# Kernel optimization log

Hardware: AMD Instinct MI355X
Metric: run time of the kernel (lower is better)

Reference implementation:

```python
import jax, jax.numpy as jnp
import numpy as np

N_NODE, NODE_DIM = 20000, 128
N_EDGE, EDGE_DIM = 40000, 16
BN_EPS = 1e-5


def _bn(x, gamma, beta):
    # training-mode BatchNorm1d: batch statistics, biased variance
    mu = jnp.mean(x, axis=0)
    var = jnp.mean((x - mu) ** 2, axis=0)
    return (x - mu) * jax.lax.rsqrt(var + BN_EPS) * gamma + beta


def setup_inputs() -> dict:
    key = jax.random.key(0)
    ks = jax.random.split(key, 16)
    D = NODE_DIM

    def lin(k, fan_in, fan_out):
        s = 1.0 / np.sqrt(fan_in)
        return jax.random.uniform(k, (fan_in, fan_out), jnp.float32, -s, s)

    inp = {
        "node": jax.random.normal(ks[0], (N_NODE, D), jnp.float32),
        "edge_index": jax.random.randint(ks[1], (N_EDGE, 2), 0, N_NODE),
        "edge": jax.random.normal(ks[2], (N_EDGE, EDGE_DIM), jnp.float32),
        "hidden": jax.random.normal(ks[3], (1, N_NODE, D), jnp.float32),
        # encoder: LinearBn(edge_dim,256) ReLU LinearBn(256,256) ReLU LinearBn(256,128) ReLU LinearBn(128,D*D)
        "W1": lin(ks[4], EDGE_DIM, 256), "g1": jnp.ones((256,)), "be1": jnp.zeros((256,)),
        "W2": lin(ks[5], 256, 256), "g2": jnp.ones((256,)), "be2": jnp.zeros((256,)),
        "W3": lin(ks[6], 256, 128), "g3": jnp.ones((128,)), "be3": jnp.zeros((128,)),
        "W4": lin(ks[7], 128, D * D), "g4": jnp.ones((D * D,)), "be4": jnp.zeros((D * D,)),
        "bias": jax.random.uniform(ks[8], (D,), jnp.float32, -1.0 / np.sqrt(D), 1.0 / np.sqrt(D)),
        # GRU weights, torch layout [3D, D]
        "W_ih": lin(ks[9], D, 3 * D).T, "W_hh": lin(ks[10], D, 3 * D).T,
        "b_ih": jax.random.uniform(ks[11], (3 * D,), jnp.float32, -1.0 / np.sqrt(D), 1.0 / np.sqrt(D)),
        "b_hh": jax.random.uniform(ks[12], (3 * D,), jnp.float32, -1.0 / np.sqrt(D), 1.0 / np.sqrt(D)),
    }
    return inp


def reference(node, edge_index, edge, hidden,
              W1, g1, be1, W2, g2, be2, W3, g3, be3, W4, g4, be4,
              bias, W_ih, W_hh, b_ih, b_hh):
    num_node, D = node.shape
    src = edge_index[:, 0]
    dst = edge_index[:, 1]

    # edge encoder -> per-edge [D, D] mixing matrix
    h = jax.nn.relu(_bn(edge @ W1, g1, be1))
    h = jax.nn.relu(_bn(h @ W2, g2, be2))
    h = jax.nn.relu(_bn(h @ W3, g3, be3))
    ew = _bn(h @ W4, g4, be4).reshape(-1, D, D)  # [E, D, D]

    # gather + per-edge 1xD @ DxD
    x_i = node[src]                               # [E, D]
    message = jnp.einsum('ed,edf->ef', x_i, ew)   # [E, D]

    # scatter-mean over destination nodes
    sums = jax.ops.segment_sum(message, dst, num_segments=num_node)
    cnt = jax.ops.segment_sum(jnp.ones((message.shape[0],), message.dtype), dst, num_segments=num_node)
    mean = sums / jnp.maximum(cnt, 1.0)[:, None]

    msg = jax.nn.relu(mean + bias)

    # GRU cell (seq_len=1, batch=num_node), torch gate order r,z,n
    h0 = hidden[0]
    gi = msg @ W_ih.T + b_ih
    gh = h0 @ W_hh.T + b_hh
    gi_r, gi_z, gi_n = jnp.split(gi, 3, axis=-1)
    gh_r, gh_z, gh_n = jnp.split(gh, 3, axis=-1)
    r = jax.nn.sigmoid(gi_r + gh_r)
    z = jax.nn.sigmoid(gi_z + gh_z)
    n = jnp.tanh(gi_n + r * gh_n)
    h1 = (1.0 - z) * n + z * h0

    return h1, h1[None]
```

## Files before the change

### kernel.cpp

```cpp
#include <hip/hip_runtime.h>
#include <cstdint>
#include <cstddef>

#define N_NODE_C 20000
#define N_EDGE_C 40000
#define BN_EPS_F 1e-5f
#define NSB 160
#define H3T_STRIDE 40064

typedef __attribute__((ext_vector_type(8))) short bf16x8;
typedef __attribute__((ext_vector_type(16))) float f32x16;

__device__ __forceinline__ ushort f2bf(float x) {
  unsigned u = __float_as_uint(x);
  unsigned r = u + 0x7fffu + ((u >> 16) & 1u);
  return (ushort)(r >> 16);
}
__device__ __forceinline__ float bf2f(ushort b) {
  return __uint_as_float(((unsigned)b) << 16);
}

__device__ __forceinline__ void gl_lds16(const ushort* g, ushort* l) {
  __builtin_amdgcn_global_load_lds(
      (const __attribute__((address_space(1))) unsigned int*)(g),
      (__attribute__((address_space(3))) unsigned int*)(l), 16, 0, 0);
}

__global__ __launch_bounds__(256) void k_transpose_gru(
    const float* __restrict__ Wih, const float* __restrict__ Whh,
    float* __restrict__ WihT, float* __restrict__ WhhT) {
  int i = blockIdx.x * 256 + threadIdx.x;
  int which = i / 49152;
  int idx = i - which * 49152;
  int k = idx / 384, o = idx - k * 384;
  float v = which ? Whh[o * 128 + k] : Wih[o * 128 + k];
  if (which) WhhT[idx] = v; else WihT[idx] = v;
}

__global__ __launch_bounds__(256) void k_edge_w1(
    const float* __restrict__ edge, const float* __restrict__ W1,
    float* __restrict__ y1) {
  __shared__ float el[16][16];
  int e0 = blockIdx.x * 16;
  int t = threadIdx.x;
  el[t >> 4][t & 15] = edge[(size_t)e0 * 16 + t];
  __syncthreads();
  float w[16];
#pragma unroll
  for (int k = 0; k < 16; ++k) w[k] = W1[k * 256 + t];
#pragma unroll 4
  for (int e = 0; e < 16; ++e) {
    float acc = 0.f;
#pragma unroll
    for (int k = 0; k < 16; ++k) acc = fmaf(el[e][k], w[k], acc);
    y1[(size_t)(e0 + e) * 256 + t] = acc;
  }
}

__global__ __launch_bounds__(256) void k_colstats(
    const float* __restrict__ y, int E, int J,
    double* __restrict__ sum, double* __restrict__ sumsq) {
  int t = threadIdx.x;
  int rpi = 256 / J;
  int col = t & (J - 1);
  int rof = t / J;
  double s = 0.0, q = 0.0;
  for (int r = blockIdx.x * rpi + rof; r < E; r += gridDim.x * rpi) {
    float v = y[(size_t)r * J + col];
    s += v;
    q += (double)v * (double)v;
  }
  atomicAdd(&sum[col], s);
  atomicAdd(&sumsq[col], q);
}

__global__ void k_finalize(const double* __restrict__ sum,
                           const double* __restrict__ sumsq,
                           const float* __restrict__ g,
                           const float* __restrict__ be,
                           float* __restrict__ a, float* __restrict__ b,
                           int J, double invE) {
  int j = threadIdx.x;
  if (j < J) {
    double mu = sum[j] * invE;
    double var = sumsq[j] * invE - mu * mu;
    float rstd = (float)(1.0 / sqrt(var + 1e-5));
    float aa = g[j] * rstd;
    a[j] = aa;
    b[j] = be[j] - (float)mu * aa;
  }
}

template <int MODE>
__global__ __launch_bounds__(256) void k_gemm(
    const float* __restrict__ A, const float* __restrict__ B,
    float* __restrict__ C, int M, int K, int N,
    const float* __restrict__ ta, const float* __restrict__ tb,
    const float* __restrict__ bias) {
  __shared__ float At[32][64];
  __shared__ float Bt[32][128];
  int mb = blockIdx.x * 64, nb = blockIdx.y * 128;
  int tid = threadIdx.x;
  int tr = tid >> 5, tc = tid & 31;
  float acc[8][4];
#pragma unroll
  for (int i = 0; i < 8; ++i)
#pragma unroll
    for (int j = 0; j < 4; ++j) acc[i][j] = 0.f;
  int arow = tid >> 2, akc = (tid & 3) * 8;
  int bkr = tid >> 3, bcol = (tid & 7) * 16;
  for (int k0 = 0; k0 < K; k0 += 32) {
    {
      int gr = mb + arow;
      float vv[8];
      if (gr < M) {
        float4 v0 = *(const float4*)&A[(size_t)gr * K + k0 + akc];
        float4 v1 = *(const float4*)&A[(size_t)gr * K + k0 + akc + 4];
        vv[0] = v0.x; vv[1] = v0.y; vv[2] = v0.z; vv[3] = v0.w;
        vv[4] = v1.x; vv[5] = v1.y; vv[6] = v1.z; vv[7] = v1.w;
      } else {
#pragma unroll
        for (int u = 0; u < 8; ++u) vv[u] = 0.f;
      }
#pragma unroll
      for (int u = 0; u < 8; ++u) {
        float x = vv[u];
        if (MODE == 1) {
          int k = k0 + akc + u;
          x = fmaxf(fmaf(x, ta[k], tb[k]), 0.f);
        }
        At[akc + u][arow] = x;
      }
    }
    {
      const float* src = &B[(size_t)(k0 + bkr) * N + nb + bcol];
      float4* d = (float4*)&Bt[bkr][bcol];
      d[0] = ((const float4*)src)[0];
      d[1] = ((const float4*)src)[1];
      d[2] = ((const float4*)src)[2];
      d[3] = ((const float4*)src)[3];
    }
    __syncthreads();
#pragma unroll 8
    for (int kk = 0; kk < 32; ++kk) {
      float4 a0 = *(float4*)&At[kk][tr * 8];
      float4 a1 = *(float4*)&At[kk][tr * 8 + 4];
      float4 b0 = *(float4*)&Bt[kk][tc * 4];
      float av[8] = {a0.x, a0.y, a0.z, a0.w, a1.x, a1.y, a1.z, a1.w};
      float bv[4] = {b0.x, b0.y, b0.z, b0.w};
#pragma unroll
      for (int i = 0; i < 8; ++i)
#pragma unroll
        for (int j = 0; j < 4; ++j)
          acc[i][j] = fmaf(av[i], bv[j], acc[i][j]);
    }
    __syncthreads();
  }
#pragma unroll
  for (int i = 0; i < 8; ++i) {
    int gr = mb + tr * 8 + i;
    if (gr < M) {
      int oc = nb + tc * 4;
      float4 o;
      o.x = acc[i][0]; o.y = acc[i][1]; o.z = acc[i][2]; o.w = acc[i][3];
      if (bias) {
        o.x += bias[oc]; o.y += bias[oc + 1];
        o.z += bias[oc + 2]; o.w += bias[oc + 3];
      }
      *(float4*)&C[(size_t)gr * N + oc] = o;
    }
  }
}

__global__ __launch_bounds__(256) void k_bnrelu_inplace(
    float* __restrict__ y, const float* __restrict__ a,
    const float* __restrict__ b, int n, int J) {
  int i = blockIdx.x * 256 + threadIdx.x;
  if (i < n) {
    int c = i & (J - 1);
    y[i] = fmaxf(fmaf(y[i], a[c], b[c]), 0.f);
  }
}

__global__ __launch_bounds__(256) void k_cov_partials(
    const float* __restrict__ h3, float* __restrict__ Spart,
    float* __restrict__ hbarP) {
  __shared__ float hl[2][128];
  int b = blockIdx.x;
  int t = threadIdx.x;
  int tr = t >> 4, tc = t & 15;
  float acc[8][8];
#pragma unroll
  for (int i = 0; i < 8; ++i)
#pragma unroll
    for (int j = 0; j < 8; ++j) acc[i][j] = 0.f;
  float cs = 0.f;
  int r0 = b * 250;
  for (int rs = 0; rs < 250; rs += 2) {
    hl[t >> 7][t & 127] = h3[(size_t)(r0 + rs + (t >> 7)) * 128 + (t & 127)];
    __syncthreads();
#pragma unroll
    for (int rr = 0; rr < 2; ++rr) {
      float a0[8], b0[8];
#pragma unroll
      for (int i = 0; i < 8; ++i) a0[i] = hl[rr][tr * 8 + i];
#pragma unroll
      for (int j = 0; j < 8; ++j) b0[j] = hl[rr][tc * 8 + j];
#pragma unroll
      for (int i = 0; i < 8; ++i)
#pragma unroll
        for (int j = 0; j < 8; ++j)
          acc[i][j] = fmaf(a0[i], b0[j], acc[i][j]);
    }
    if (t < 128) cs += hl[0][t] + hl[1][t];
    __syncthreads();
  }
  float* sp = &Spart[(size_t)b * 16384];
#pragma unroll
  for (int i = 0; i < 8; ++i)
#pragma unroll
    for (int j = 0; j < 8; j += 4) {
      float4 o;
      o.x = acc[i][j]; o.y = acc[i][j + 1];
      o.z = acc[i][j + 2]; o.w = acc[i][j + 3];
      *(float4*)&sp[(tr * 8 + i) * 128 + tc * 8 + j] = o;
    }
  if (t < 128) hbarP[b * 128 + t] = cs;
}

__global__ void k_hbar(const float* __restrict__ hbarP,
                       double* __restrict__ hbarD, float* __restrict__ hbarF) {
  int t = threadIdx.x;
  double s = 0.0;
  for (int b = 0; b < NSB; ++b) s += (double)hbarP[b * 128 + t];
  s *= (1.0 / 40000.0);
  hbarD[t] = s;
  hbarF[t] = (float)s;
}

__global__ __launch_bounds__(256) void k_cov(
    const float* __restrict__ Spart, const double* __restrict__ hbarD,
    float* __restrict__ Cov) {
  int i = blockIdx.x * 256 + threadIdx.x;
  int k = i >> 7, l = i & 127;
  double s = 0.0;
  for (int b = 0; b < NSB; ++b) s += (double)Spart[(size_t)b * 16384 + i];
  Cov[i] = (float)(s * (1.0 / 40000.0) - hbarD[k] * hbarD[l]);
}

__global__ __launch_bounds__(256) void k_covW4(
    const float* __restrict__ Cov, const float* __restrict__ W4,
    float* __restrict__ U) {
  __shared__ float cl[8][128];
  int bk = blockIdx.x & 15, bj = blockIdx.x >> 4;
  int k0 = bk * 8, j0 = bj * 2048;
  int t = threadIdx.x;
  {
    float4 v = *(const float4*)&Cov[(size_t)(k0 + (t >> 5)) * 128 + (t & 31) * 4];
    *(float4*)&cl[t >> 5][(t & 31) * 4] = v;
  }
  __syncthreads();
  for (int ji = 0; ji < 8; ++ji) {
    int j = j0 + ji * 256 + t;
    float acc[8];
#pragma unroll
    for (int i = 0; i < 8; ++i) acc[i] = 0.f;
#pragma unroll 4
    for (int l = 0; l < 128; ++l) {
      float w = W4[(size_t)l * 16384 + j];
#pragma unroll
      for (int i = 0; i < 8; ++i) acc[i] = fmaf(cl[i][l], w, acc[i]);
    }
#pragma unroll
    for (int i = 0; i < 8; ++i) U[(size_t)(k0 + i) * 16384 + j] = acc[i];
  }
}

__global__ __launch_bounds__(256) void k_a4nb4(
    const float* __restrict__ W4, const float* __restrict__ U,
    const float* __restrict__ hbarF, const float* __restrict__ g4,
    const float* __restrict__ be4, float* __restrict__ a4,
    float* __restrict__ nb4) {
  __shared__ float hb[128];
  int t = threadIdx.x;
  if (t < 128) hb[t] = hbarF[t];
  __syncthreads();
  int j = blockIdx.x * 256 + t;
  float macc = 0.f, vacc = 0.f;
#pragma unroll 4
  for (int k = 0; k < 128; ++k) {
    float w = W4[(size_t)k * 16384 + j];
    macc = fmaf(hb[k], w, macc);
    vacc = fmaf(w, U[(size_t)k * 16384 + j], vacc);
  }
  float aa = g4[j] * (1.0f / sqrtf(vacc + BN_EPS_F));
  a4[j] = aa;
  nb4[j] = be4[j] - macc * aa;
}

__global__ __launch_bounds__(256) void k_split_node(
    const float* __restrict__ node, ushort* __restrict__ nH,
    ushort* __restrict__ nL) {
  int i = blockIdx.x * 256 + threadIdx.x;
  int base = i * 4;
  float4 v = *(const float4*)&node[base];
  ushort4 h, lo;
  float x;
  x = v.x; h.x = f2bf(x); lo.x = f2bf(x - bf2f(h.x));
  x = v.y; h.y = f2bf(x); lo.y = f2bf(x - bf2f(h.y));
  x = v.z; h.z = f2bf(x); lo.z = f2bf(x - bf2f(h.z));
  x = v.w; h.w = f2bf(x); lo.w = f2bf(x - bf2f(h.w));
  *(ushort4*)&nH[base] = h;
  *(ushort4*)&nL[base] = lo;
}

__global__ __launch_bounds__(256) void k_h3T(const float* __restrict__ y3,
                                             float* __restrict__ h3T) {
  __shared__ float tile[32][33];
  int bx = blockIdx.x;
  int by = blockIdx.y;
  int tx = threadIdx.x & 31, ty = threadIdx.x >> 5;
#pragma unroll
  for (int i = 0; i < 4; ++i) {
    int e = bx * 32 + ty + 8 * i;
    float v = (e < 40000) ? y3[(size_t)e * 128 + by * 32 + tx] : 0.f;
    tile[ty + 8 * i][tx] = v;
  }
  __syncthreads();
#pragma unroll
  for (int i = 0; i < 4; ++i) {
    int kk = by * 32 + ty + 8 * i;
    h3T[(size_t)kk * H3T_STRIDE + bx * 32 + tx] = tile[tx][ty + 8 * i];
  }
}

__global__ __launch_bounds__(256) void k_buildB2(
    const float* __restrict__ W4, const float* __restrict__ a4,
    const float* __restrict__ nb4, ushort* __restrict__ B2) {
  int tid = blockIdx.x * 256 + threadIdx.x;
  int k = tid >> 14;
  int rem = tid & 16383;
  int H = rem >> 13;
  int rem2 = rem & 8191;
  int j = rem2 & 7;
  int lane = (rem2 >> 3) & 63;
  int cgg = (rem2 >> 9) & 1;
  int dstep = rem2 >> 10;
  int d = dstep * 16 + (lane >> 5) * 8 + j;
  int f = H * 64 + cgg * 32 + (lane & 31);
  int df = d * 128 + f;
  float v;
  if (k < 128) v = W4[(size_t)k * 16384 + df] * a4[df];
  else v = nb4[df];
  ushort hi = f2bf(v);
  ushort lo = f2bf(v - bf2f(hi));
  size_t base = ((size_t)(k * 2 + H)) * 16384 +
                (size_t)((dstep * 2 + cgg) * 2) * 512 + lane * 8 + j;
  B2[base] = hi;
  B2[base + 512] = lo;
}

__global__ __launch_bounds__(512) void k_biggemm3(
    const ushort* __restrict__ nodeH, const ushort* __restrict__ B2,
    const float* __restrict__ h3T, const int* __restrict__ eidx,
    float* __restrict__ msum, float* __restrict__ cnt) {
  __shared__ ushort Bl[2][8192];
  __shared__ int sidx[128], didx[128];
  const int t = threadIdx.x;
  const int e0 = blockIdx.x * 128;
  const int H = blockIdx.y;
  const int KZ = blockIdx.z;
  const int K0 = KZ ? 65 : 0;
  const int KN = KZ ? 64 : 65;
  const int w = t >> 6;
  const int l = t & 63;
  const int rg = w >> 1;
  const int cg = w & 1;
  const int dg = l >> 5;

  if (t < 256) {
    int e = e0 + (t >> 1);
    int v = (e < 40000) ? eidx[(size_t)e * 2 + (t & 1)] : 0;
    if (t & 1) didx[t >> 1] = v; else sidx[t >> 1] = v;
  }
  {
    const size_t cb = (size_t)(K0 * 2 + H) * 16384;
#pragma unroll
    for (int j = 0; j < 2; ++j) {
      int flat = t + j * 512;
      gl_lds16(B2 + cb + (size_t)(flat >> 6) * 1024 + (flat & 63) * 8,
               &Bl[0][flat * 8]);
    }
  }
  __syncthreads();

  const int myrow = rg * 32 + (l & 31);
  const int esrc = sidx[myrow];
  bf16x8 xh[8];
  {
    const ushort* ph = nodeH + (size_t)esrc * 128 + dg * 8;
#pragma unroll
    for (int d2 = 0; d2 < 8; ++d2) xh[d2] = *(const bf16x8*)(ph + d2 * 16);
  }

  f32x16 msg;
#pragma unroll
  for (int r = 0; r < 16; ++r) msg[r] = 0.f;

  for (int ki = 0; ki < KN; ++ki) {
    const int kc = K0 + ki;
    const int buf = ki & 1;
    if (ki + 1 < KN) {
      const size_t cb = (size_t)((kc + 1) * 2 + H) * 16384;
#pragma unroll
      for (int j = 0; j < 2; ++j) {
        int flat = t + j * 512;
        gl_lds16(B2 + cb + (size_t)(flat >> 6) * 1024 + (flat & 63) * 8,
                 &Bl[buf ^ 1][flat * 8]);
      }
    }
    float4 hv[4];
    if (kc < 128) {
      const float* hb = h3T + (size_t)kc * H3T_STRIDE + e0 + rg * 32 + 4 * dg;
#pragma unroll
      for (int q = 0; q < 4; ++q) hv[q] = *(const float4*)(hb + q * 8);
    } else {
#pragma unroll
      for (int q = 0; q < 4; ++q) hv[q] = make_float4(1.f, 1.f, 1.f, 1.f);
    }
    f32x16 u;
#pragma unroll
    for (int r = 0; r < 16; ++r) u[r] = 0.f;
    const ushort* bbase = &Bl[buf][0];
#pragma unroll
    for (int d2 = 0; d2 < 8; ++d2) {
      bf16x8 bh = *(const bf16x8*)(bbase + (d2 * 2 + cg) * 512 + l * 8);
      u = __builtin_amdgcn_mfma_f32_32x32x16_bf16(xh[d2], bh, u, 0, 0, 0);
    }
#pragma unroll
    for (int r = 0; r < 16; ++r) {
      float hval = ((const float*)&hv[r >> 2])[r & 3];
      msg[r] = fmaf(hval, u[r], msg[r]);
    }
    __syncthreads();
  }

  const int fbase = H * 64 + cg * 32 + (l & 31);
#pragma unroll
  for (int r = 0; r < 16; ++r) {
    int lrow = rg * 32 + (r & 3) + 8 * (r >> 2) + 4 * dg;
    int ge = e0 + lrow;
    if (ge < 40000)
      atomicAdd(&msum[(size_t)didx[lrow] * 128 + fbase], msg[r]);
  }
  if (KZ == 0 && H == 0 && t < 128) {
    int ge = e0 + t;
    if (ge < 40000) atomicAdd(&cnt[didx[t]], 1.0f);
  }
}

__global__ __launch_bounds__(256) void k_msg(
    const float* __restrict__ msum, const float* __restrict__ cnt,
    const float* __restrict__ bias, float* __restrict__ msg) {
  int i = blockIdx.x * 256 + threadIdx.x;
  int nn = i >> 7, f = i & 127;
  float m = msum[i] / fmaxf(cnt[nn], 1.0f);
  msg[i] = fmaxf(m + bias[f], 0.f);
}

__global__ __launch_bounds__(256) void k_gru(
    const float* __restrict__ gi, const float* __restrict__ gh,
    const float* __restrict__ h0, float* __restrict__ out) {
  int i = blockIdx.x * 256 + threadIdx.x;
  int nn = i >> 7, f = i & 127;
  size_t base = (size_t)nn * 384;
  float ir = gi[base + f], hr = gh[base + f];
  float iz = gi[base + 128 + f], hz = gh[base + 128 + f];
  float in_ = gi[base + 256 + f], hn = gh[base + 256 + f];
  float r = 1.f / (1.f + expf(-(ir + hr)));
  float z = 1.f / (1.f + expf(-(iz + hz)));
  float n = tanhf(in_ + r * hn);
  float h1 = (1.f - z) * n + z * h0[i];
  out[i] = h1;
  out[2560000 + i] = h1;
}

extern "C" void kernel_launch(void* const* d_in, const int* in_sizes, int n_in,
                              void* d_out, int out_size, void* d_ws,
                              size_t ws_size, hipStream_t stream) {
  (void)in_sizes; (void)n_in; (void)out_size; (void)ws_size;
  const float* node = (const float*)d_in[0];
  const int* eidx = (const int*)d_in[1];
  const float* edge = (const float*)d_in[2];
  const float* hidden = (const float*)d_in[3];
  const float* W1 = (const float*)d_in[4];
  const float* g1 = (const float*)d_in[5];
  const float* be1 = (const float*)d_in[6];
  const float* W2 = (const float*)d_in[7];
  const float* g2 = (const float*)d_in[8];
  const float* be2 = (const float*)d_in[9];
  const float* W3 = (const float*)d_in[10];
  const float* g3 = (const float*)d_in[11];
  const float* be3 = (const float*)d_in[12];
  const float* W4 = (const float*)d_in[13];
  const float* g4 = (const float*)d_in[14];
  const float* be4 = (const float*)d_in[15];
  const float* bias = (const float*)d_in[16];
  const float* Wih = (const float*)d_in[17];
  const float* Whh = (const float*)d_in[18];
  const float* bih = (const float*)d_in[19];
  const float* bhh = (const float*)d_in[20];
  float* out = (float*)d_out;

  double* d64 = (double*)d_ws;
  double* sum1 = d64 + 0;
  double* sq1 = d64 + 256;
  double* sum2 = d64 + 512;
  double* sq2 = d64 + 768;
  double* sum3 = d64 + 1024;
  double* sq3 = d64 + 1152;
  double* hbarD = d64 + 1280;
  float* F = (float*)(d64 + 1536);

  size_t o = 0;
  float* y1 = F + o;   o += 10240000;
  float* y2 = F + o;   o += 10240000;
  float* y3 = F + o;   o += 5120000;
  float* B2f = F + o;  o += 2113536;
  float* msum = F + o; o += 2560000;
  float* cnt = F + o;  o += 20000;
  float* msg = F + o;  o += 2560000;
  float* WihT = F + o; o += 49152;
  float* WhhT = F + o; o += 49152;
  float* Cov = F + o;  o += 16384;
  float* a4 = F + o;   o += 16384;
  float* nb4 = F + o;  o += 16384;
  float* a1 = F + o;   o += 256;
  float* b1 = F + o;   o += 256;
  float* a2 = F + o;   o += 256;
  float* b2 = F + o;   o += 256;
  float* a3 = F + o;   o += 128;
  float* b3 = F + o;   o += 128;
  float* hbarF = F + o; o += 128;
  float* Spart = y1;
  float* U = y1 + 2621440;
  float* gi = y1 + 2560000;
  float* h3T = y2;
  float* gh = y2;
  float* hbarP = y2 + 7680000;
  ushort* nodeH = (ushort*)msg;
  ushort* nodeL = ((ushort*)msg) + 2560000;
  ushort* B2 = (ushort*)B2f;

  hipMemsetAsync(d_ws, 0, 12288, stream);
  hipMemsetAsync(msum, 0, (2560000 + 20000) * sizeof(float), stream);

  k_transpose_gru<<<384, 256, 0, stream>>>(Wih, Whh, WihT, WhhT);
  k_split_node<<<2500, 256, 0, stream>>>(node, nodeH, nodeL);

  k_edge_w1<<<2500, 256, 0, stream>>>(edge, W1, y1);
  k_colstats<<<256, 256, 0, stream>>>(y1, 40000, 256, sum1, sq1);
  k_finalize<<<1, 256, 0, stream>>>(sum1, sq1, g1, be1, a1, b1, 256, 1.0 / 40000.0);
  k_gemm<1><<<dim3(625, 2), 256, 0, stream>>>(y1, W2, y2, 40000, 256, 256, a1, b1, nullptr);
  k_colstats<<<256, 256, 0, stream>>>(y2, 40000, 256, sum2, sq2);
  k_finalize<<<1, 256, 0, stream>>>(sum2, sq2, g2, be2, a2, b2, 256, 1.0 / 40000.0);
  k_gemm<1><<<dim3(625, 1), 256, 0, stream>>>(y2, W3, y3, 40000, 256, 128, a2, b2, nullptr);
  k_colstats<<<256, 256, 0, stream>>>(y3, 40000, 128, sum3, sq3);
  k_finalize<<<1, 256, 0, stream>>>(sum3, sq3, g3, be3, a3, b3, 128, 1.0 / 40000.0);
  k_bnrelu_inplace<<<20000, 256, 0, stream>>>(y3, a3, b3, 5120000, 128);

  k_h3T<<<dim3(1252, 4), 256, 0, stream>>>(y3, h3T);

  k_cov_partials<<<NSB, 256, 0, stream>>>(y3, Spart, hbarP);
  k_hbar<<<1, 128, 0, stream>>>(hbarP, hbarD, hbarF);
  k_cov<<<64, 256, 0, stream>>>(Spart, hbarD, Cov);
  k_covW4<<<128, 256, 0, stream>>>(Cov, W4, U);
  k_a4nb4<<<64, 256, 0, stream>>>(W4, U, hbarF, g4, be4, a4, nb4);
  k_buildB2<<<8256, 256, 0, stream>>>(W4, a4, nb4, B2);

  k_biggemm3<<<dim3(313, 2, 2), 512, 0, stream>>>(nodeH, B2, h3T, eidx,
                                                  msum, cnt);

  k_msg<<<10000, 256, 0, stream>>>(msum, cnt, bias, msg);
  k_gemm<0><<<dim3(313, 3), 256, 0, stream>>>(msg, WihT, gi, 20000, 128, 384, nullptr, nullptr, bih);
  k_gemm<0><<<dim3(313, 3), 256, 0, stream>>>(hidden, WhhT, gh, 20000, 128, 384, nullptr, nullptr, bhh);
  k_gru<<<10000, 256, 0, stream>>>(gi, gh, hidden, out);
}
```

Baseline: 875.8 us.

## Move encoder and GRU GEMMs to split-bf16 MFMA, drop low plane in big GEMM

Replaces the fp32 SIMT tiled GEMMs (encoder layers 2 and 3, GRU input and hidden projections) with MFMA 32x32x16 bf16 kernels. These use hi/lo bf16 splitting of both operands (three MFMAs per k-step) to keep near-fp32 accuracy, with new pack kernels that fuse the BN+ReLU prologue into the A split. It also removes the low-precision correction plane from the B2 edge-weight operand of the big message GEMM, halving its load traffic at some accuracy cost. The extra pack passes add memory traffic and launches.

```diff
diff --git a/kernel.cpp b/kernel.cpp
--- a/kernel.cpp
+++ b/kernel.cpp
@@ -24,17 +24,6 @@
   __builtin_amdgcn_global_load_lds(
       (const __attribute__((address_space(1))) unsigned int*)(g),
       (__attribute__((address_space(3))) unsigned int*)(l), 16, 0, 0);
-}
-
-__global__ __launch_bounds__(256) void k_transpose_gru(
-    const float* __restrict__ Wih, const float* __restrict__ Whh,
-    float* __restrict__ WihT, float* __restrict__ WhhT) {
-  int i = blockIdx.x * 256 + threadIdx.x;
-  int which = i / 49152;
-  int idx = i - which * 49152;
-  int k = idx / 384, o = idx - k * 384;
-  float v = which ? Whh[o * 128 + k] : Wih[o * 128 + k];
-  if (which) WhhT[idx] = v; else WihT[idx] = v;
 }
 
 __global__ __launch_bounds__(256) void k_edge_w1(
@@ -88,87 +77,6 @@
     float aa = g[j] * rstd;
     a[j] = aa;
     b[j] = be[j] - (float)mu * aa;
-  }
-}
-
-template <int MODE>
-__global__ __launch_bounds__(256) void k_gemm(
-    const float* __restrict__ A, const float* __restrict__ B,
-    float* __restrict__ C, int M, int K, int N,
-    const float* __restrict__ ta, const float* __restrict__ tb,
-    const float* __restrict__ bias) {
-  __shared__ float At[32][64];
-  __shared__ float Bt[32][128];
-  int mb = blockIdx.x * 64, nb = blockIdx.y * 128;
-  int tid = threadIdx.x;
-  int tr = tid >> 5, tc = tid & 31;
-  float acc[8][4];
-#pragma unroll
-  for (int i = 0; i < 8; ++i)
-#pragma unroll
-    for (int j = 0; j < 4; ++j) acc[i][j] = 0.f;
-  int arow = tid >> 2, akc = (tid & 3) * 8;
-  int bkr = tid >> 3, bcol = (tid & 7) * 16;
-  for (int k0 = 0; k0 < K; k0 += 32) {
-    {
-      int gr = mb + arow;
-      float vv[8];
-      if (gr < M) {
-        float4 v0 = *(const float4*)&A[(size_t)gr * K + k0 + akc];
-        float4 v1 = *(const float4*)&A[(size_t)gr * K + k0 + akc + 4];
-        vv[0] = v0.x; vv[1] = v0.y; vv[2] = v0.z; vv[3] = v0.w;
-        vv[4] = v1.x; vv[5] = v1.y; vv[6] = v1.z; vv[7] = v1.w;
-      } else {
-#pragma unroll
-        for (int u = 0; u < 8; ++u) vv[u] = 0.f;
-      }
-#pragma unroll
-      for (int u = 0; u < 8; ++u) {
-        float x = vv[u];
-        if (MODE == 1) {
-          int k = k0 + akc + u;
-          x = fmaxf(fmaf(x, ta[k], tb[k]), 0.f);
-        }
-        At[akc + u][arow] = x;
-      }
-    }
-    {
-      const float* src = &B[(size_t)(k0 + bkr) * N + nb + bcol];
-      float4* d = (float4*)&Bt[bkr][bcol];
-      d[0] = ((const float4*)src)[0];
-      d[1] = ((const float4*)src)[1];
-      d[2] = ((const float4*)src)[2];
-      d[3] = ((const float4*)src)[3];
-    }
-    __syncthreads();
-#pragma unroll 8
-    for (int kk = 0; kk < 32; ++kk) {
-      float4 a0 = *(float4*)&At[kk][tr * 8];
-      float4 a1 = *(float4*)&At[kk][tr * 8 + 4];
-      float4 b0 = *(float4*)&Bt[kk][tc * 4];
-      float av[8] = {a0.x, a0.y, a0.z, a0.w, a1.x, a1.y, a1.z, a1.w};
-      float bv[4] = {b0.x, b0.y, b0.z, b0.w};
-#pragma unroll
-      for (int i = 0; i < 8; ++i)
-#pragma unroll
-        for (int j = 0; j < 4; ++j)
-          acc[i][j] = fmaf(av[i], bv[j], acc[i][j]);
-    }
-    __syncthreads();
-  }
-#pragma unroll
-  for (int i = 0; i < 8; ++i) {
-    int gr = mb + tr * 8 + i;
-    if (gr < M) {
-      int oc = nb + tc * 4;
-      float4 o;
-      o.x = acc[i][0]; o.y = acc[i][1]; o.z = acc[i][2]; o.w = acc[i][3];
-      if (bias) {
-        o.x += bias[oc]; o.y += bias[oc + 1];
-        o.z += bias[oc + 2]; o.w += bias[oc + 3];
-      }
-      *(float4*)&C[(size_t)gr * N + oc] = o;
-    }
   }
 }
 
@@ -352,12 +260,110 @@
   float v;
   if (k < 128) v = W4[(size_t)k * 16384 + df] * a4[df];
   else v = nb4[df];
+  B2[(size_t)(k * 2 + H) * 8192 + rem2] = f2bf(v);
+}
+
+template <int TRANSPOSED>
+__global__ __launch_bounds__(256) void k_packW(
+    const float* __restrict__ W, int Nd32, int ldw, ushort* __restrict__ out) {
+  int tid = blockIdx.x * 256 + threadIdx.x;
+  int within = tid & 511;
+  int g = tid >> 9;
+  int nt = g % Nd32, kt = g / Nd32;
+  int lane = within >> 3, j = within & 7;
+  int k = kt * 16 + (lane >> 5) * 8 + j;
+  int n = nt * 32 + (lane & 31);
+  float v = TRANSPOSED ? W[(size_t)n * ldw + k] : W[(size_t)k * ldw + n];
   ushort hi = f2bf(v);
   ushort lo = f2bf(v - bf2f(hi));
-  size_t base = ((size_t)(k * 2 + H)) * 16384 +
-                (size_t)((dstep * 2 + cgg) * 2) * 512 + lane * 8 + j;
-  B2[base] = hi;
-  B2[base + 512] = lo;
+  out[((size_t)g * 2 + 0) * 512 + within] = hi;
+  out[((size_t)g * 2 + 1) * 512 + within] = lo;
+}
+
+template <int MODE>
+__global__ __launch_bounds__(256) void k_splitA(
+    const float* __restrict__ A, int M, int Kd16,
+    const float* __restrict__ ta, const float* __restrict__ tb,
+    ushort* __restrict__ out) {
+  int tid = blockIdx.x * 256 + threadIdx.x;
+  int lane = tid & 63;
+  int g = tid >> 6;
+  int kt = g % Kd16, m32 = g / Kd16;
+  int row = m32 * 32 + (lane & 31);
+  int kbase = kt * 16 + (lane >> 5) * 8;
+  float v[8];
+  if (row < M) {
+    const float* src = A + (size_t)row * (Kd16 * 16) + kbase;
+    float4 v0 = ((const float4*)src)[0];
+    float4 v1 = ((const float4*)src)[1];
+    v[0] = v0.x; v[1] = v0.y; v[2] = v0.z; v[3] = v0.w;
+    v[4] = v1.x; v[5] = v1.y; v[6] = v1.z; v[7] = v1.w;
+  } else {
+#pragma unroll
+    for (int u = 0; u < 8; ++u) v[u] = 0.f;
+  }
+  ushort hi[8], lo[8];
+#pragma unroll
+  for (int u = 0; u < 8; ++u) {
+    float x = v[u];
+    if (MODE == 1) {
+      int k = kbase + u;
+      x = fmaxf(fmaf(x, ta[k], tb[k]), 0.f);
+    }
+    hi[u] = f2bf(x);
+    lo[u] = f2bf(x - bf2f(hi[u]));
+  }
+  size_t obase = ((size_t)g * 2) * 512 + lane * 8;
+  *(ushort4*)&out[obase] = make_ushort4(hi[0], hi[1], hi[2], hi[3]);
+  *(ushort4*)&out[obase + 4] = make_ushort4(hi[4], hi[5], hi[6], hi[7]);
+  *(ushort4*)&out[obase + 512] = make_ushort4(lo[0], lo[1], lo[2], lo[3]);
+  *(ushort4*)&out[obase + 516] = make_ushort4(lo[4], lo[5], lo[6], lo[7]);
+}
+
+template <int KD16, int HAS_BIAS>
+__global__ __launch_bounds__(512) void k_mfgemm(
+    const ushort* __restrict__ Apk, const ushort* __restrict__ Bpk,
+    float* __restrict__ C, int M, int Nd32, const float* __restrict__ bias) {
+  __shared__ ushort Bl[KD16 * 4 * 512];
+  const int t = threadIdx.x;
+  const int mb = blockIdx.x, nb = blockIdx.y;
+  const int w = t >> 6, l = t & 63;
+  const int rg = w >> 1, cg = w & 1, dg = l >> 5;
+  constexpr int passes = (KD16 * 4 * 64) / 512;
+#pragma unroll
+  for (int p = 0; p < passes; ++p) {
+    int flat = t + p * 512;
+    int blk = flat >> 6;
+    int off = (flat & 63) * 8;
+    int kt = blk >> 2, cgg = (blk >> 1) & 1, plane = blk & 1;
+    size_t srcb = ((size_t)(kt * Nd32 + nb * 2 + cgg) * 2 + plane) * 512 + off;
+    gl_lds16(Bpk + srcb, &Bl[blk * 512 + off]);
+  }
+  __syncthreads();
+  f32x16 u;
+#pragma unroll
+  for (int r = 0; r < 16; ++r) u[r] = 0.f;
+  const int m32base = mb * 4 + rg;
+#pragma unroll
+  for (int kt = 0; kt < KD16; ++kt) {
+    const ushort* ap = Apk + ((size_t)(m32base * KD16 + kt) * 2) * 512 + l * 8;
+    bf16x8 ah = *(const bf16x8*)ap;
+    bf16x8 al = *(const bf16x8*)(ap + 512);
+    const ushort* bp = &Bl[(kt * 4 + cg * 2) * 512 + l * 8];
+    bf16x8 bh = *(const bf16x8*)bp;
+    bf16x8 bl2 = *(const bf16x8*)(bp + 512);
+    u = __builtin_amdgcn_mfma_f32_32x32x16_bf16(ah, bh, u, 0, 0, 0);
+    u = __builtin_amdgcn_mfma_f32_32x32x16_bf16(ah, bl2, u, 0, 0, 0);
+    u = __builtin_amdgcn_mfma_f32_32x32x16_bf16(al, bh, u, 0, 0, 0);
+  }
+  const int N = Nd32 * 32;
+  const int col = nb * 64 + cg * 32 + (l & 31);
+  const float bv = HAS_BIAS ? bias[col] : 0.f;
+#pragma unroll
+  for (int r = 0; r < 16; ++r) {
+    int row = mb * 128 + rg * 32 + (r & 3) + 8 * (r >> 2) + 4 * dg;
+    if (row < M) C[(size_t)row * N + col] = u[r] + bv;
+  }
 }
 
 __global__ __launch_bounds__(512) void k_biggemm3(
@@ -384,12 +390,11 @@
     if (t & 1) didx[t >> 1] = v; else sidx[t >> 1] = v;
   }
   {
-    const size_t cb = (size_t)(K0 * 2 + H) * 16384;
-#pragma unroll
-    for (int j = 0; j < 2; ++j) {
-      int flat = t + j * 512;
-      gl_lds16(B2 + cb + (size_t)(flat >> 6) * 1024 + (flat & 63) * 8,
-               &Bl[0][flat * 8]);
+    const size_t cb = (size_t)(K0 * 2 + H) * 8192;
+#pragma unroll
+    for (int jj = 0; jj < 2; ++jj) {
+      int flat = t + jj * 512;
+      gl_lds16(B2 + cb + (size_t)flat * 8, &Bl[0][flat * 8]);
     }
   }
   __syncthreads();
@@ -411,12 +416,11 @@
     const int kc = K0 + ki;
     const int buf = ki & 1;
     if (ki + 1 < KN) {
-      const size_t cb = (size_t)((kc + 1) * 2 + H) * 16384;
-#pragma unroll
-      for (int j = 0; j < 2; ++j) {
-        int flat = t + j * 512;
-        gl_lds16(B2 + cb + (size_t)(flat >> 6) * 1024 + (flat & 63) * 8,
-                 &Bl[buf ^ 1][flat * 8]);
+      const size_t cb = (size_t)((kc + 1) * 2 + H) * 8192;
+#pragma unroll
+      for (int jj = 0; jj < 2; ++jj) {
+        int flat = t + jj * 512;
+        gl_lds16(B2 + cb + (size_t)flat * 8, &Bl[buf ^ 1][flat * 8]);
       }
     }
     float4 hv[4];
@@ -523,55 +527,69 @@
   float* F = (float*)(d64 + 1536);
 
   size_t o = 0;
-  float* y1 = F + o;   o += 10240000;
-  float* y2 = F + o;   o += 10240000;
-  float* y3 = F + o;   o += 5120000;
-  float* B2f = F + o;  o += 2113536;
-  float* msum = F + o; o += 2560000;
-  float* cnt = F + o;  o += 20000;
-  float* msg = F + o;  o += 2560000;
-  float* WihT = F + o; o += 49152;
-  float* WhhT = F + o; o += 49152;
-  float* Cov = F + o;  o += 16384;
-  float* a4 = F + o;   o += 16384;
-  float* nb4 = F + o;  o += 16384;
-  float* a1 = F + o;   o += 256;
-  float* b1 = F + o;   o += 256;
-  float* a2 = F + o;   o += 256;
-  float* b2 = F + o;   o += 256;
-  float* a3 = F + o;   o += 128;
-  float* b3 = F + o;   o += 128;
+  float* S1 = F + o;    o += 10320000;
+  float* S2 = F + o;    o += 10320000;
+  float* S3 = F + o;    o += 5150000;
+  float* B2f = F + o;   o += 1056768;
+  float* msum = F + o;  o += 2560000;
+  float* cnt = F + o;   o += 20000;
+  float* msgb = F + o;  o += 2560000;
+  float* Wihpkf = F + o; o += 49152;
+  float* Whhpkf = F + o; o += 49152;
+  float* W2pkf = F + o;  o += 65536;
+  float* W3pkf = F + o;  o += 32768;
+  float* Cov = F + o;   o += 16384;
+  float* a4 = F + o;    o += 16384;
+  float* nb4 = F + o;   o += 16384;
+  float* a1 = F + o;    o += 256;
+  float* b1 = F + o;    o += 256;
+  float* a2 = F + o;    o += 256;
+  float* b2 = F + o;    o += 256;
+  float* a3 = F + o;    o += 128;
+  float* b3 = F + o;    o += 128;
   float* hbarF = F + o; o += 128;
-  float* Spart = y1;
-  float* U = y1 + 2621440;
-  float* gi = y1 + 2560000;
-  float* h3T = y2;
-  float* gh = y2;
-  float* hbarP = y2 + 7680000;
-  ushort* nodeH = (ushort*)msg;
-  ushort* nodeL = ((ushort*)msg) + 2560000;
+  ushort* nodeH = (ushort*)msgb;
+  ushort* nodeL = ((ushort*)msgb) + 2560000;
   ushort* B2 = (ushort*)B2f;
+  ushort* W2pk = (ushort*)W2pkf;
+  ushort* W3pk = (ushort*)W3pkf;
+  ushort* Wihpk = (ushort*)Wihpkf;
+  ushort* Whhpk = (ushort*)Whhpkf;
+  ushort* A2pk = (ushort*)S2;
+  float* h3T = S1;
+  float* Spart = S1 + 5200000;
+  float* hbarP = S1 + 7900000;
+  float* U = S1 + 7950000;
+  float* gh = S1;
+  float* gi = S2;
+  ushort* msgpk = (ushort*)S3;
+  ushort* hidpk = ((ushort*)S3) + 2572288 * 2;
 
   hipMemsetAsync(d_ws, 0, 12288, stream);
   hipMemsetAsync(msum, 0, (2560000 + 20000) * sizeof(float), stream);
 
-  k_transpose_gru<<<384, 256, 0, stream>>>(Wih, Whh, WihT, WhhT);
   k_split_node<<<2500, 256, 0, stream>>>(node, nodeH, nodeL);
-
-  k_edge_w1<<<2500, 256, 0, stream>>>(edge, W1, y1);
-  k_colstats<<<256, 256, 0, stream>>>(y1, 40000, 256, sum1, sq1);
+  k_packW<0><<<256, 256, 0, stream>>>(W2, 8, 256, W2pk);
+  k_packW<0><<<128, 256, 0, stream>>>(W3, 4, 128, W3pk);
+  k_packW<1><<<192, 256, 0, stream>>>(Wih, 12, 128, Wihpk);
+  k_packW<1><<<192, 256, 0, stream>>>(Whh, 12, 128, Whhpk);
+
+  k_edge_w1<<<2500, 256, 0, stream>>>(edge, W1, S1);
+  k_colstats<<<256, 256, 0, stream>>>(S1, 40000, 256, sum1, sq1);
   k_finalize<<<1, 256, 0, stream>>>(sum1, sq1, g1, be1, a1, b1, 256, 1.0 / 40000.0);
-  k_gemm<1><<<dim3(625, 2), 256, 0, stream>>>(y1, W2, y2, 40000, 256, 256, a1, b1, nullptr);
-  k_colstats<<<256, 256, 0, stream>>>(y2, 40000, 256, sum2, sq2);
+  k_splitA<1><<<5008, 256, 0, stream>>>(S1, 40000, 16, a1, b1, A2pk);
+  k_mfgemm<16, 0><<<dim3(313, 4), 512, 0, stream>>>(A2pk, W2pk, S1, 40000, 8, nullptr);
+  k_colstats<<<256, 256, 0, stream>>>(S1, 40000, 256, sum2, sq2);
   k_finalize<<<1, 256, 0, stream>>>(sum2, sq2, g2, be2, a2, b2, 256, 1.0 / 40000.0);
-  k_gemm<1><<<dim3(625, 1), 256, 0, stream>>>(y2, W3, y3, 40000, 256, 128, a2, b2, nullptr);
-  k_colstats<<<256, 256, 0, stream>>>(y3, 40000, 128, sum3, sq3);
+  k_splitA<1><<<5008, 256, 0, stream>>>(S1, 40000, 16, a2, b2, A2pk);
+  k_mfgemm<16, 0><<<dim3(313, 2), 512, 0, stream>>>(A2pk, W3pk, S3, 40000, 4, nullptr);
+  k_colstats<<<256, 256, 0, stream>>>(S3, 40000, 128, sum3, sq3);
   k_finalize<<<1, 256, 0, stream>>>(sum3, sq3, g3, be3, a3, b3, 128, 1.0 / 40000.0);
-  k_bnrelu_inplace<<<20000, 256, 0, stream>>>(y3, a3, b3, 5120000, 128);
-
-  k_h3T<<<dim3(1252, 4), 256, 0, stream>>>(y3, h3T);
-
-  k_cov_partials<<<NSB, 256, 0, stream>>>(y3, Spart, hbarP);
+  k_bnrelu_inplace<<<20000, 256, 0, stream>>>(S3, a3, b3, 5120000, 128);
+
+  k_h3T<<<dim3(1252, 4), 256, 0, stream>>>(S3, h3T);
+
+  k_cov_partials<<<NSB, 256, 0, stream>>>(S3, Spart, hbarP);
   k_hbar<<<1, 128, 0, stream>>>(hbarP, hbarD, hbarF);
   k_cov<<<64, 256, 0, stream>>>(Spart, hbarD, Cov);
   k_covW4<<<128, 256, 0, stream>>>(Cov, W4, U);
@@ -581,8 +599,10 @@
   k_biggemm3<<<dim3(313, 2, 2), 512, 0, stream>>>(nodeH, B2, h3T, eidx,
                                                   msum, cnt);
 
-  k_msg<<<10000, 256, 0, stream>>>(msum, cnt, bias, msg);
-  k_gemm<0><<<dim3(313, 3), 256, 0, stream>>>(msg, WihT, gi, 20000, 128, 384, nullptr, nullptr, bih);
-  k_gemm<0><<<dim3(313, 3), 256, 0, stream>>>(hidden, WhhT, gh, 20000, 128, 384, nullptr, nullptr, bhh);
+  k_msg<<<10000, 256, 0, stream>>>(msum, cnt, bias, msgb);
+  k_splitA<0><<<1256, 256, 0, stream>>>(msgb, 20000, 8, nullptr, nullptr, msgpk);
+  k_splitA<0><<<1256, 256, 0, stream>>>(hidden, 20000, 8, nullptr, nullptr, hidpk);
+  k_mfgemm<8, 1><<<dim3(157, 6), 512, 0, stream>>>(msgpk, Wihpk, gi, 20000, 12, bih);
+  k_mfgemm<8, 1><<<dim3(157, 6), 512, 0, stream>>>(hidpk, Whhpk, gh, 20000, 12, bhh);
   k_gru<<<10000, 256, 0, stream>>>(gi, gh, hidden, out);
 }
```

After: 844.2 us. -3.6%, faster.
